# Kernel tuning notes

Measured on AMD Instinct MI355X. Metric: run time of the kernel, lower is better.

## Reference

```python
import jax, jax.numpy as jnp
import numpy as np

B, N, E, D, H, O = 4, 10000, 160000, 128, 4, 64
NEG_SLOPE = 0.2  # PyG GATConv default


def setup_inputs() -> dict:
    key = jax.random.key(0)
    ks = jax.random.split(key, 9)
    x = jax.random.normal(ks[0], (B, N, D), jnp.float32)
    edge_index = jax.random.randint(ks[1], (2, E), 0, N, dtype=jnp.int64)
    edge_attr = jax.random.uniform(ks[2], (E,), jnp.float32)
    W_src = jax.random.normal(ks[3], (D, H, O), jnp.float32) * (1.0 / np.sqrt(D))
    att_src = jax.random.normal(ks[4], (H, O), jnp.float32) * 0.1
    att_dst = jax.random.normal(ks[5], (H, O), jnp.float32) * 0.1
    W_edge = jax.random.normal(ks[6], (H, O), jnp.float32) * 0.1  # lin_edge weight for edge_dim=1
    att_edge = jax.random.normal(ks[7], (H, O), jnp.float32) * 0.1
    bias = jnp.zeros((O,), jnp.float32)
    return {"x": x, "edge_index": edge_index, "edge_attr": edge_attr,
            "W_src": W_src, "att_src": att_src, "att_dst": att_dst,
            "W_edge": W_edge, "att_edge": att_edge, "bias": bias}


def reference(x, edge_index, edge_attr, W_src, att_src, att_dst, W_edge, att_edge, bias):
    src, dst = edge_index[0], edge_index[1]
    # shared linear projection (PyG non-bipartite GATConv): [B,N,H,O]
    h = jnp.einsum('bnd,dho->bnho', x, W_src)
    a_src = jnp.einsum('bnho,ho->bnh', h, att_src)  # [B,N,H]
    a_dst = jnp.einsum('bnho,ho->bnh', h, att_dst)  # [B,N,H]
    # edge feature projection (edge_dim=1): [E,H]
    a_edge = edge_attr[:, None] * jnp.einsum('ho,ho->h', W_edge, att_edge)[None, :]
    # attention logits per edge: [B,E,H]
    alpha = a_src[:, src] + a_dst[:, dst] + a_edge[None]
    alpha = jax.nn.leaky_relu(alpha, NEG_SLOPE)
    # segment softmax over destination nodes; segment ops need axis 0 = E
    alpha_t = jnp.transpose(alpha, (1, 0, 2))  # [E,B,H]
    m = jax.ops.segment_max(alpha_t, dst, num_segments=N)  # [N,B,H]
    m = jnp.where(jnp.isfinite(m), m, 0.0)
    p = jnp.exp(alpha_t - m[dst])
    s = jax.ops.segment_sum(p, dst, num_segments=N)
    w = p / jnp.maximum(s[dst], jnp.asarray(1e-16, p.dtype))  # [E,B,H]
    # weighted messages from source nodes, scatter-add into destinations
    msg = w[..., None] * jnp.transpose(h[:, src], (1, 0, 2, 3))  # [E,B,H,O]
    out = jax.ops.segment_sum(msg, dst, num_segments=N)  # [N,B,H,O]
    out = out.mean(axis=2) + bias  # concat=False -> mean over heads, [N,B,O]
    return jnp.transpose(out, (1, 0, 2))  # [B,N,O]
```

## Files before the change

kernel.cpp:

```cpp
#include <hip/hip_runtime.h>
#include <hip/hip_fp16.h>
#include <math.h>

constexpr int B_  = 4;
constexpr int N_  = 10000;
constexpr int E_  = 160000;
constexpr int D_  = 128;
constexpr int H_  = 4;
constexpr int O_  = 64;
constexpr float NEG_SLOPE = 0.2f;
constexpr int CAP = 64;
constexpr int PLACE_BLOCKS = E_ / 256;
constexpr int GEMM_BLOCKS  = (B_ * N_) / 64;

using half8   = __attribute__((ext_vector_type(8))) _Float16;
using half2v  = __attribute__((ext_vector_type(2))) _Float16;
using f32x4   = __attribute__((ext_vector_type(4))) float;
using ushort8v = __attribute__((ext_vector_type(8))) unsigned short;

static __device__ __forceinline__ unsigned short f2h(float f) {
    return __half_as_ushort(__float2half(f));
}
static __device__ __forceinline__ float h2f(unsigned short u) {
    return __half2float(__ushort_as_half(u));
}

#if __has_builtin(__builtin_amdgcn_fdot2)
#define FDOT2(a, b, c) __builtin_amdgcn_fdot2((a), (b), (c), false)
#else
static __device__ __forceinline__ float FDOT2(half2v a, half2v b, float c) {
    return c + (float)a[0] * (float)b[0] + (float)a[1] * (float)b[1];
}
#endif

__global__ __launch_bounds__(256) void k_prep(
    const float* __restrict__ Wsrc, const float* __restrict__ att_src,
    const float* __restrict__ att_dst,
    const float* __restrict__ W_edge, const float* __restrict__ att_edge,
    unsigned short* __restrict__ W1t, unsigned short* __restrict__ Vt,
    int* __restrict__ deg, float* __restrict__ c)
{
    const int d = blockIdx.x;
    const int t = threadIdx.x;
    const int h = t >> 6;

    for (int i = d * 256 + t; i < N_; i += 128 * 256) deg[i] = 0;

    const float wv = Wsrc[(size_t)d * 256 + t];
    const int cc = ((t & 63) << 2) | h;
    W1t[(size_t)cc * 128 + d] = f2h(wv);

    float vs = wv * att_src[t];
    float vd = wv * att_dst[t];
#pragma unroll
    for (int off = 32; off > 0; off >>= 1) {
        vs += __shfl_down(vs, off, 64);
        vd += __shfl_down(vd, off, 64);
    }
    if ((t & 63) == 0) {
        Vt[h * 128 + d]       = f2h(vs);
        Vt[(4 + h) * 128 + d] = f2h(vd);
    }
    if (d == 1) {
#pragma unroll
        for (int k = 0; k < 4; ++k) Vt[1024 + k * 256 + t] = 0;
    }

    if (d == 0) {
        float v = W_edge[t] * att_edge[t];
#pragma unroll
        for (int off = 32; off > 0; off >>= 1) v += __shfl_down(v, off, 64);
        if ((t & 63) == 0) c[h] = v;
    }
}

__global__ __launch_bounds__(256) void k_gemm(
    const float* __restrict__ x, const int* __restrict__ ei,
    const float* __restrict__ eattr,
    const unsigned short* __restrict__ W1t, const unsigned short* __restrict__ Vt,
    unsigned short* __restrict__ hbw, float* __restrict__ asrc, float* __restrict__ adst,
    int* __restrict__ deg, int2* __restrict__ srcea)
{
    constexpr int APAD = 136;
    __shared__ uint4 SHq[2112];
    unsigned short* A0 = (unsigned short*)SHq;
    unsigned short* A1 = (unsigned short*)SHq + 4352;
    unsigned short* Cb = (unsigned short*)SHq + 8704;

    const int t = threadIdx.x;

    if (blockIdx.x < PLACE_BLOCKS) {
        const int e = blockIdx.x * 256 + t;
        const int dstn = ei[E_ + e];
        const int r = atomicAdd(&deg[dstn], 1);
        srcea[dstn * CAP + r] = make_int2(ei[e], __float_as_int(eattr[e]));
        return;
    }

    const int w = t >> 6;
    const int lane = t & 63;
    const int i = lane & 15;
    const int q = lane >> 4;
    const size_t rowbase = (size_t)(blockIdx.x - PLACE_BLOCKS) * 64;

    const float4* xg = (const float4*)(x + rowbase * D_);
    float4 xr0[4], xr1[4];
#pragma unroll
    for (int it = 0; it < 4; ++it) xr0[it] = xg[it * 256 + t];
#pragma unroll
    for (int it = 0; it < 4; ++it) xr1[it] = xg[1024 + it * 256 + t];

    half8 breg[4][4];
#pragma unroll
    for (int ks = 0; ks < 4; ++ks)
#pragma unroll
        for (int ctl = 0; ctl < 4; ++ctl) {
            const size_t boff = (size_t)((w * 4 + ctl) * 16 + i) * 128 + ks * 32 + q * 8;
            breg[ks][ctl] = *(const half8*)&W1t[boff];
        }
    half8 vreg[4];
    if (w < 2) {
#pragma unroll
        for (int ks = 0; ks < 4; ++ks)
            vreg[ks] = *(const half8*)&Vt[i * 128 + ks * 32 + q * 8];
    }

#pragma unroll
    for (int it = 0; it < 4; ++it) {
        const int idx = it * 256 + t;
        const int row = idx >> 5;
        const int c4  = idx & 31;
        ushort4 h1;
        h1.x = f2h(xr0[it].x); h1.y = f2h(xr0[it].y);
        h1.z = f2h(xr0[it].z); h1.w = f2h(xr0[it].w);
        *(ushort4*)&A0[row * APAD + c4 * 4] = h1;
    }
    __syncthreads();

    f32x4 acc0[2][4];
#pragma unroll
    for (int tl = 0; tl < 2; ++tl)
#pragma unroll
        for (int ctl = 0; ctl < 4; ++ctl) acc0[tl][ctl] = (f32x4){0.f, 0.f, 0.f, 0.f};
    f32x4 accV0 = (f32x4){0.f, 0.f, 0.f, 0.f};

#pragma unroll
    for (int ks = 0; ks < 4; ++ks) {
        const int a0off = i * APAD + ks * 32 + q * 8;
        const int a1off = (16 + i) * APAD + ks * 32 + q * 8;
        half8 at0 = *(const half8*)&A0[a0off];
        half8 at1 = *(const half8*)&A0[a1off];
#pragma unroll
        for (int ctl = 0; ctl < 4; ++ctl) {
            acc0[0][ctl] = __builtin_amdgcn_mfma_f32_16x16x32_f16(at0, breg[ks][ctl], acc0[0][ctl], 0, 0, 0);
            acc0[1][ctl] = __builtin_amdgcn_mfma_f32_16x16x32_f16(at1, breg[ks][ctl], acc0[1][ctl], 0, 0, 0);
        }
        if (w < 2) {
            const half8 atV = (w == 0) ? at0 : at1;
            accV0 = __builtin_amdgcn_mfma_f32_16x16x32_f16(atV, vreg[ks], accV0, 0, 0, 0);
        }
    }

#pragma unroll
    for (int it = 0; it < 4; ++it) {
        const int idx = it * 256 + t;
        const int row = idx >> 5;
        const int c4  = idx & 31;
        ushort4 h1;
        h1.x = f2h(xr1[it].x); h1.y = f2h(xr1[it].y);
        h1.z = f2h(xr1[it].z); h1.w = f2h(xr1[it].w);
        *(ushort4*)&A1[row * APAD + c4 * 4] = h1;
    }

    if (w < 2 && i < 8) {
#pragma unroll
        for (int r = 0; r < 4; ++r) {
            const int row = w * 16 + q * 4 + r;
            const size_t rg = rowbase + row;
            if (i < 4) asrc[rg * 4 + i]       = accV0[r];
            else       adst[rg * 4 + (i - 4)] = accV0[r];
        }
    }
    __syncthreads();

    f32x4 acc1[2][4];
#pragma unroll
    for (int tl = 0; tl < 2; ++tl)
#pragma unroll
        for (int ctl = 0; ctl < 4; ++ctl) acc1[tl][ctl] = (f32x4){0.f, 0.f, 0.f, 0.f};
    f32x4 accV1 = (f32x4){0.f, 0.f, 0.f, 0.f};

#pragma unroll
    for (int ks = 0; ks < 4; ++ks) {
        const int a0off = i * APAD + ks * 32 + q * 8;
        const int a1off = (16 + i) * APAD + ks * 32 + q * 8;
        half8 at0 = *(const half8*)&A1[a0off];
        half8 at1 = *(const half8*)&A1[a1off];
#pragma unroll
        for (int ctl = 0; ctl < 4; ++ctl) {
            acc1[0][ctl] = __builtin_amdgcn_mfma_f32_16x16x32_f16(at0, breg[ks][ctl], acc1[0][ctl], 0, 0, 0);
            acc1[1][ctl] = __builtin_amdgcn_mfma_f32_16x16x32_f16(at1, breg[ks][ctl], acc1[1][ctl], 0, 0, 0);
        }
        if (w < 2) {
            const half8 atV = (w == 0) ? at0 : at1;
            accV1 = __builtin_amdgcn_mfma_f32_16x16x32_f16(atV, vreg[ks], accV1, 0, 0, 0);
        }
    }

#pragma unroll
    for (int tl = 0; tl < 2; ++tl) {
#pragma unroll
        for (int ctl = 0; ctl < 4; ++ctl) {
            const int col = (w * 4 + ctl) * 16 + i;
            const int chnk = col >> 3;
            const int within = col & 7;
#pragma unroll
            for (int r = 0; r < 4; ++r) {
                const int row = tl * 16 + q * 4 + r;
                const int s = chnk ^ row;
                Cb[row * 256 + s * 8 + within] = f2h(acc0[tl][ctl][r]);
            }
        }
    }

    if (w < 2 && i < 8) {
#pragma unroll
        for (int r = 0; r < 4; ++r) {
            const int row = w * 16 + q * 4 + r;
            const size_t rg = rowbase + 32 + row;
            if (i < 4) asrc[rg * 4 + i]       = accV1[r];
            else       adst[rg * 4 + (i - 4)] = accV1[r];
        }
    }
    __syncthreads();

    {
        const int chnk = t & 31;
#pragma unroll
        for (int k = 0; k < 4; ++k) {
            const int row = k * 8 + (t >> 5);
            const int s = chnk ^ row;
            const uint4 v = *(const uint4*)&Cb[row * 256 + s * 8];
            *(uint4*)&hbw[(rowbase + row) * 256 + chnk * 8] = v;
        }
    }
    __syncthreads();

#pragma unroll
    for (int tl = 0; tl < 2; ++tl) {
#pragma unroll
        for (int ctl = 0; ctl < 4; ++ctl) {
            const int col = (w * 4 + ctl) * 16 + i;
            const int chnk = col >> 3;
            const int within = col & 7;
#pragma unroll
            for (int r = 0; r < 4; ++r) {
                const int row = tl * 16 + q * 4 + r;
                const int s = chnk ^ row;
                Cb[row * 256 + s * 8 + within] = f2h(acc1[tl][ctl][r]);
            }
        }
    }
    __syncthreads();

    {
        const int chnk = t & 31;
#pragma unroll
        for (int k = 0; k < 4; ++k) {
            const int row = k * 8 + (t >> 5);
            const int s = chnk ^ row;
            const uint4 v = *(const uint4*)&Cb[row * 256 + s * 8];
            *(uint4*)&hbw[(rowbase + 32 + row) * 256 + chnk * 8] = v;
        }
    }
}

__global__ __launch_bounds__(256) void k_agg(
    const int* __restrict__ deg, const int2* __restrict__ srcea,
    const float* __restrict__ asrc, const float* __restrict__ adst,
    const float* __restrict__ cvec, const unsigned short* __restrict__ hbu,
    const float* __restrict__ bias, float* __restrict__ out)
{
    __shared__ uint4 jS[4][64];

    const int b    = blockIdx.x & 3;
    const int g    = blockIdx.x >> 2;
    const int wave = threadIdx.x >> 6;
    const int lane = threadIdx.x & 63;
    const int dst  = g * 4 + wave;

    const int dg    = deg[dst];
    const int ebase = dst * CAP;

    const float4 ad = *(const float4*)&adst[((size_t)b * N_ + dst) * 4];
    const float4 cc = *(const float4*)cvec;

    const bool valid = lane < dg;
    const int2 rec = srcea[ebase + (valid ? lane : 0)];
    const int   srcl = valid ? rec.x : 0;
    const float ea   = __int_as_float(rec.y);
    const float4 as = *(const float4*)&asrc[((size_t)b * N_ + srcl) * 4];
    float4 al;
    al.x = as.x + ad.x + ea * cc.x;
    al.y = as.y + ad.y + ea * cc.y;
    al.z = as.z + ad.z + ea * cc.z;
    al.w = as.w + ad.w + ea * cc.w;
    al.x = al.x > 0.f ? al.x : NEG_SLOPE * al.x;
    al.y = al.y > 0.f ? al.y : NEG_SLOPE * al.y;
    al.z = al.z > 0.f ? al.z : NEG_SLOPE * al.z;
    al.w = al.w > 0.f ? al.w : NEG_SLOPE * al.w;
    float q0 = valid ? __expf(al.x) : 0.f;
    float q1 = valid ? __expf(al.y) : 0.f;
    float q2 = valid ? __expf(al.z) : 0.f;
    float q3 = valid ? __expf(al.w) : 0.f;
    const float px = q0, py = q1, pz = q2, pw = q3;

#pragma unroll
    for (int off = 32; off > 0; off >>= 1) {
        q0 += __shfl_xor(q0, off, 64);
        q1 += __shfl_xor(q1, off, 64);
        q2 += __shfl_xor(q2, off, 64);
        q3 += __shfl_xor(q3, off, 64);
    }
    const float i0 = 1.f / fmaxf(q0, 1e-16f);
    const float i1 = 1.f / fmaxf(q1, 1e-16f);
    const float i2 = 1.f / fmaxf(q2, 1e-16f);
    const float i3 = 1.f / fmaxf(q3, 1e-16f);

    union { half2v h; unsigned u; } u01, u23;
    u01.h[0] = (_Float16)(px * i0); u01.h[1] = (_Float16)(py * i1);
    u23.h[0] = (_Float16)(pz * i2); u23.h[1] = (_Float16)(pw * i3);
    jS[wave][lane] = make_uint4((unsigned)((b * N_ + srcl) << 8), u01.u, u23.u, 0u);
    __builtin_amdgcn_wave_barrier();

    const int half = lane >> 5;
    const int ol   = (lane & 31) * 8;

    float a0[4] = {0.f, 0.f, 0.f, 0.f};
    float a1[4] = {0.f, 0.f, 0.f, 0.f};

    for (int j = 0; j < dg; j += 8) {
#pragma unroll
        for (int u = 0; u < 4; ++u) {
            const int idx = j + 2 * u + half;
            const uint4 e4 = jS[wave][idx];
            const ushort8v hh = *(const ushort8v*)&hbu[(size_t)e4.x + ol];
            union { ushort8v s; half2v h[4]; } H; H.s = hh;
            union { unsigned u; half2v h; } p01, p23;
            p01.u = e4.y; p23.u = e4.z;
            a0[u] = FDOT2(H.h[0], p01.h, a0[u]);
            a0[u] = FDOT2(H.h[1], p23.h, a0[u]);
            a1[u] = FDOT2(H.h[2], p01.h, a1[u]);
            a1[u] = FDOT2(H.h[3], p23.h, a1[u]);
        }
    }

    float t0 = (a0[0] + a0[1]) + (a0[2] + a0[3]);
    float t1 = (a1[0] + a1[1]) + (a1[2] + a1[3]);
    t0 += __shfl_xor(t0, 32, 64);
    t1 += __shfl_xor(t1, 32, 64);

    if (lane < 32) {
        const float2 bs = *(const float2*)&bias[lane * 2];
        float2 res;
        res.x = 0.25f * t0 + bs.x;
        res.y = 0.25f * t1 + bs.y;
        *(float2*)&out[((size_t)b * N_ + dst) * O_ + lane * 2] = res;
    }
}

extern "C" void kernel_launch(void* const* d_in, const int* in_sizes, int n_in,
                              void* d_out, int out_size, void* d_ws, size_t ws_size,
                              hipStream_t stream)
{
    (void)in_sizes; (void)n_in; (void)out_size; (void)ws_size;
    const float* x        = (const float*)d_in[0];
    const int*   ei       = (const int*)d_in[1];
    const float* eattr    = (const float*)d_in[2];
    const float* Wsrc     = (const float*)d_in[3];
    const float* att_src  = (const float*)d_in[4];
    const float* att_dst  = (const float*)d_in[5];
    const float* W_edge   = (const float*)d_in[6];
    const float* att_edge = (const float*)d_in[7];
    const float* bias     = (const float*)d_in[8];
    float* out = (float*)d_out;

    char* w = (char*)d_ws;
    auto take = [&](size_t bytes) { char* p = w; w += (bytes + 15) & ~size_t(15); return p; };
    unsigned short* hb   = (unsigned short*)take((size_t)B_ * N_ * O_ * H_ * 2);
    float* asrc    = (float*)take((size_t)B_ * N_ * H_ * 4);
    float* adst    = (float*)take((size_t)B_ * N_ * H_ * 4);
    float* c       = (float*)take(4 * 4);
    unsigned short* W1t = (unsigned short*)take((size_t)256 * 128 * 2);
    unsigned short* Vt  = (unsigned short*)take((size_t)16 * 128 * 2);
    int* deg       = (int*)take((size_t)N_ * 4);
    int2* srcea    = (int2*)take((size_t)N_ * CAP * 8);

    hipLaunchKernelGGL(k_prep, dim3(128), dim3(256), 0, stream,
                       Wsrc, att_src, att_dst, W_edge, att_edge,
                       W1t, Vt, deg, c);
    hipLaunchKernelGGL(k_gemm, dim3(PLACE_BLOCKS + GEMM_BLOCKS), dim3(256), 0, stream,
                       x, ei, eattr, W1t, Vt, hb, asrc, adst, deg, srcea);
    hipLaunchKernelGGL(k_agg, dim3(N_ / 4 * B_), dim3(256), 0, stream,
                       deg, srcea, asrc, adst, c, hb, bias, out);
}
```

Before: 133.9 us.

## Process four destination nodes per wave in aggregation kernel

Each wave in k_agg now handles four destination nodes instead of one, interleaving their gathers and softmax reductions so more independent loads are in flight. The grid shrinks by four times and the loop runs to the maximum degree among the four nodes, stepping four edges at a time. This aims to raise memory-level parallelism for the gather of h rows. In exchange it uses more registers and LDS per wave, and some lanes do padded work when degrees differ.

```diff
diff --git a/kernel.cpp b/kernel.cpp
--- a/kernel.cpp
+++ b/kernel.cpp
@@ -32,6 +32,7 @@
     return c + (float)a[0] * (float)b[0] + (float)a[1] * (float)b[1];
 }
 #endif
+
 
 __global__ __launch_bounds__(256) void k_prep(
     const float* __restrict__ Wsrc, const float* __restrict__ att_src,
@@ -281,91 +282,132 @@
     const float* __restrict__ cvec, const unsigned short* __restrict__ hbu,
     const float* __restrict__ bias, float* __restrict__ out)
 {
-    __shared__ uint4 jS[4][64];
+    __shared__ uint4 jS[4][4][64];
 
     const int b    = blockIdx.x & 3;
     const int g    = blockIdx.x >> 2;
     const int wave = threadIdx.x >> 6;
     const int lane = threadIdx.x & 63;
-    const int dst  = g * 4 + wave;
-
-    const int dg    = deg[dst];
-    const int ebase = dst * CAP;
-
-    const float4 ad = *(const float4*)&adst[((size_t)b * N_ + dst) * 4];
+
     const float4 cc = *(const float4*)cvec;
 
-    const bool valid = lane < dg;
-    const int2 rec = srcea[ebase + (valid ? lane : 0)];
-    const int   srcl = valid ? rec.x : 0;
-    const float ea   = __int_as_float(rec.y);
-    const float4 as = *(const float4*)&asrc[((size_t)b * N_ + srcl) * 4];
-    float4 al;
-    al.x = as.x + ad.x + ea * cc.x;
-    al.y = as.y + ad.y + ea * cc.y;
-    al.z = as.z + ad.z + ea * cc.z;
-    al.w = as.w + ad.w + ea * cc.w;
-    al.x = al.x > 0.f ? al.x : NEG_SLOPE * al.x;
-    al.y = al.y > 0.f ? al.y : NEG_SLOPE * al.y;
-    al.z = al.z > 0.f ? al.z : NEG_SLOPE * al.z;
-    al.w = al.w > 0.f ? al.w : NEG_SLOPE * al.w;
-    float q0 = valid ? __expf(al.x) : 0.f;
-    float q1 = valid ? __expf(al.y) : 0.f;
-    float q2 = valid ? __expf(al.z) : 0.f;
-    float q3 = valid ? __expf(al.w) : 0.f;
-    const float px = q0, py = q1, pz = q2, pw = q3;
-
-#pragma unroll
-    for (int off = 32; off > 0; off >>= 1) {
-        q0 += __shfl_xor(q0, off, 64);
-        q1 += __shfl_xor(q1, off, 64);
-        q2 += __shfl_xor(q2, off, 64);
-        q3 += __shfl_xor(q3, off, 64);
-    }
-    const float i0 = 1.f / fmaxf(q0, 1e-16f);
-    const float i1 = 1.f / fmaxf(q1, 1e-16f);
-    const float i2 = 1.f / fmaxf(q2, 1e-16f);
-    const float i3 = 1.f / fmaxf(q3, 1e-16f);
-
-    union { half2v h; unsigned u; } u01, u23;
-    u01.h[0] = (_Float16)(px * i0); u01.h[1] = (_Float16)(py * i1);
-    u23.h[0] = (_Float16)(pz * i2); u23.h[1] = (_Float16)(pw * i3);
-    jS[wave][lane] = make_uint4((unsigned)((b * N_ + srcl) << 8), u01.u, u23.u, 0u);
+    int  dstv[4], dgv[4], srcv[4];
+    int2 recv[4];
+    float pv[4][4], qv[4][4];
+
+#pragma unroll
+    for (int k = 0; k < 4; ++k) {
+        dstv[k] = g * 16 + k * 4 + wave;
+        dgv[k]  = deg[dstv[k]];
+    }
+#pragma unroll
+    for (int k = 0; k < 4; ++k) {
+        const bool v = lane < dgv[k];
+        recv[k] = srcea[dstv[k] * CAP + (v ? lane : 0)];
+    }
+
+#pragma unroll
+    for (int k = 0; k < 4; ++k) {
+        const bool v = lane < dgv[k];
+        srcv[k] = v ? recv[k].x : 0;
+        const float ea = __int_as_float(recv[k].y);
+        const float4 ad = *(const float4*)&adst[((size_t)b * N_ + dstv[k]) * 4];
+        const float4 as = *(const float4*)&asrc[((size_t)b * N_ + srcv[k]) * 4];
+        float4 al;
+        al.x = as.x + ad.x + ea * cc.x;
+        al.y = as.y + ad.y + ea * cc.y;
+        al.z = as.z + ad.z + ea * cc.z;
+        al.w = as.w + ad.w + ea * cc.w;
+        al.x = al.x > 0.f ? al.x : NEG_SLOPE * al.x;
+        al.y = al.y > 0.f ? al.y : NEG_SLOPE * al.y;
+        al.z = al.z > 0.f ? al.z : NEG_SLOPE * al.z;
+        al.w = al.w > 0.f ? al.w : NEG_SLOPE * al.w;
+        qv[k][0] = v ? __expf(al.x) : 0.f;
+        qv[k][1] = v ? __expf(al.y) : 0.f;
+        qv[k][2] = v ? __expf(al.z) : 0.f;
+        qv[k][3] = v ? __expf(al.w) : 0.f;
+        pv[k][0] = qv[k][0]; pv[k][1] = qv[k][1];
+        pv[k][2] = qv[k][2]; pv[k][3] = qv[k][3];
+    }
+
+#pragma unroll
+    for (int off = 32; off > 0; off >>= 1)
+#pragma unroll
+        for (int k = 0; k < 4; ++k) {
+            qv[k][0] += __shfl_xor(qv[k][0], off, 64);
+            qv[k][1] += __shfl_xor(qv[k][1], off, 64);
+            qv[k][2] += __shfl_xor(qv[k][2], off, 64);
+            qv[k][3] += __shfl_xor(qv[k][3], off, 64);
+        }
+
+#pragma unroll
+    for (int k = 0; k < 4; ++k) {
+        const float i0 = 1.f / fmaxf(qv[k][0], 1e-16f);
+        const float i1 = 1.f / fmaxf(qv[k][1], 1e-16f);
+        const float i2 = 1.f / fmaxf(qv[k][2], 1e-16f);
+        const float i3 = 1.f / fmaxf(qv[k][3], 1e-16f);
+        union { half2v h; unsigned u; } u01, u23;
+        u01.h[0] = (_Float16)(pv[k][0] * i0); u01.h[1] = (_Float16)(pv[k][1] * i1);
+        u23.h[0] = (_Float16)(pv[k][2] * i2); u23.h[1] = (_Float16)(pv[k][3] * i3);
+        jS[wave][k][lane] = make_uint4((unsigned)((b * N_ + srcv[k]) << 8), u01.u, u23.u, 0u);
+    }
     __builtin_amdgcn_wave_barrier();
 
     const int half = lane >> 5;
     const int ol   = (lane & 31) * 8;
 
-    float a0[4] = {0.f, 0.f, 0.f, 0.f};
-    float a1[4] = {0.f, 0.f, 0.f, 0.f};
-
-    for (int j = 0; j < dg; j += 8) {
-#pragma unroll
-        for (int u = 0; u < 4; ++u) {
+    float a0[4][2], a1[4][2];
+#pragma unroll
+    for (int k = 0; k < 4; ++k)
+#pragma unroll
+        for (int u = 0; u < 2; ++u) { a0[k][u] = 0.f; a1[k][u] = 0.f; }
+
+    int dgM = dgv[0] > dgv[1] ? dgv[0] : dgv[1];
+    dgM = dgM > dgv[2] ? dgM : dgv[2];
+    dgM = dgM > dgv[3] ? dgM : dgv[3];
+
+    for (int j = 0; j < dgM; j += 4) {
+#pragma unroll
+        for (int u = 0; u < 2; ++u) {
             const int idx = j + 2 * u + half;
-            const uint4 e4 = jS[wave][idx];
-            const ushort8v hh = *(const ushort8v*)&hbu[(size_t)e4.x + ol];
-            union { ushort8v s; half2v h[4]; } H; H.s = hh;
-            union { unsigned u; half2v h; } p01, p23;
-            p01.u = e4.y; p23.u = e4.z;
-            a0[u] = FDOT2(H.h[0], p01.h, a0[u]);
-            a0[u] = FDOT2(H.h[1], p23.h, a0[u]);
-            a1[u] = FDOT2(H.h[2], p01.h, a1[u]);
-            a1[u] = FDOT2(H.h[3], p23.h, a1[u]);
-        }
-    }
-
-    float t0 = (a0[0] + a0[1]) + (a0[2] + a0[3]);
-    float t1 = (a1[0] + a1[1]) + (a1[2] + a1[3]);
-    t0 += __shfl_xor(t0, 32, 64);
-    t1 += __shfl_xor(t1, 32, 64);
-
-    if (lane < 32) {
-        const float2 bs = *(const float2*)&bias[lane * 2];
-        float2 res;
-        res.x = 0.25f * t0 + bs.x;
-        res.y = 0.25f * t1 + bs.y;
-        *(float2*)&out[((size_t)b * N_ + dst) * O_ + lane * 2] = res;
+#pragma unroll
+            for (int k = 0; k < 4; ++k) {
+                const uint4 e = jS[wave][k][idx];
+                const ushort8v hh = *(const ushort8v*)&hbu[(size_t)e.x + ol];
+                union { ushort8v s; half2v h[4]; } H; H.s = hh;
+                union { unsigned uu; half2v h; } p01, p23;
+                p01.uu = e.y; p23.uu = e.z;
+                a0[k][u] = FDOT2(H.h[0], p01.h, a0[k][u]);
+                a0[k][u] = FDOT2(H.h[1], p23.h, a0[k][u]);
+                a1[k][u] = FDOT2(H.h[2], p01.h, a1[k][u]);
+                a1[k][u] = FDOT2(H.h[3], p23.h, a1[k][u]);
+            }
+        }
+    }
+
+    float t0[4], t1[4];
+#pragma unroll
+    for (int k = 0; k < 4; ++k) {
+        t0[k] = a0[k][0] + a0[k][1];
+        t1[k] = a1[k][0] + a1[k][1];
+        t0[k] += __shfl_xor(t0[k], 32, 64);
+        t1[k] += __shfl_xor(t1[k], 32, 64);
+    }
+
+    {
+        const int lo = lane & 31;
+        const float2 bs = *(const float2*)&bias[lo * 2];
+        const int   dA  = half ? dstv[2] : dstv[0];
+        const int   dB  = half ? dstv[3] : dstv[1];
+        const float sA0 = half ? t0[2] : t0[0];
+        const float sA1 = half ? t1[2] : t1[0];
+        const float sB0 = half ? t0[3] : t0[1];
+        const float sB1 = half ? t1[3] : t1[1];
+        float2 rA, rB;
+        rA.x = 0.25f * sA0 + bs.x;  rA.y = 0.25f * sA1 + bs.y;
+        rB.x = 0.25f * sB0 + bs.x;  rB.y = 0.25f * sB1 + bs.y;
+        *(float2*)&out[((size_t)b * N_ + dA) * O_ + lo * 2] = rA;
+        *(float2*)&out[((size_t)b * N_ + dB) * O_ + lo * 2] = rB;
     }
 }
 
@@ -401,6 +443,6 @@
                        W1t, Vt, deg, c);
     hipLaunchKernelGGL(k_gemm, dim3(PLACE_BLOCKS + GEMM_BLOCKS), dim3(256), 0, stream,
                        x, ei, eattr, W1t, Vt, hb, asrc, adst, deg, srcea);
-    hipLaunchKernelGGL(k_agg, dim3(N_ / 4 * B_), dim3(256), 0, stream,
+    hipLaunchKernelGGL(k_agg, dim3(N_ / 16 * B_), dim3(256), 0, stream,
                        deg, srcea, asrc, adst, c, hb, bias, out);
 }
```

After: 134.2 us. About the same (+0.2%).
